# Kernel optimization log

Measured on AMD Instinct MI355X. Metric: run time of the kernel, lower is better.

## Reference

```python
import jax, jax.numpy as jnp
import numpy as np

NY = NX = 512
NSHOT = 4
NSRC = 2
NREC = 64
NT = 32
DX = 5.0          # grid spacing (m)
DT = 5e-4         # time step (s)
PML_WIDTH = 20
PML_FREQ = 25.0
MAX_VEL = 3500.0
C1, C2 = 9.0 / 8.0, -1.0 / 24.0  # 4th-order staggered FD coefficients


def _shift(p, axis, o, n):
    idx = [slice(None)] * p.ndim
    idx[axis] = slice(2 + o, 2 + o + n)
    return p[tuple(idx)]


def diff_plus(f, axis, d):
    # forward staggered derivative: value at half point between i and i+1
    n = f.shape[axis]
    pad = [(0, 0)] * f.ndim
    pad[axis] = (2, 2)
    p = jnp.pad(f, pad)
    return (C1 * (_shift(p, axis, 1, n) - _shift(p, axis, 0, n))
            + C2 * (_shift(p, axis, 2, n) - _shift(p, axis, -1, n))) / d


def diff_minus(f, axis, d):
    # backward staggered derivative
    n = f.shape[axis]
    pad = [(0, 0)] * f.ndim
    pad[axis] = (2, 2)
    p = jnp.pad(f, pad)
    return (C1 * (_shift(p, axis, 0, n) - _shift(p, axis, -1, n))
            + C2 * (_shift(p, axis, 1, n) - _shift(p, axis, -2, n))) / d


def pml_profiles(n):
    # C-PML coefficients a, b along one axis
    x = jnp.arange(n, dtype=jnp.float32)
    w = float(PML_WIDTH)
    frac = jnp.clip(jnp.maximum((w - x) / w, (x - (n - 1 - w)) / w), 0.0, 1.0)
    sigma = (3.0 * MAX_VEL * np.float32(np.log(1000.0)) / (2.0 * w * DX)) * frac ** 2
    alpha = np.float32(np.pi * PML_FREQ)
    b = jnp.exp(-(sigma + alpha) * DT)
    a = sigma / (sigma + alpha) * (b - 1.0)
    return a, b


def elastic_forward(lamb, mu, buoyancy, source_amplitudes_y,
                    source_locations_y, receiver_locations_y):
    ny, nx = lamb.shape
    nshot, nsrc, nt = source_amplitudes_y.shape
    ay, by = pml_profiles(ny)
    ax, bx = pml_profiles(nx)
    ay, by = ay[None, :, None], by[None, :, None]
    ax, bx = ax[None, None, :], bx[None, None, :]
    lam2mu = lamb + 2.0 * mu

    sb = jnp.arange(nshot)[:, None]
    sy, sx = source_locations_y[..., 0], source_locations_y[..., 1]
    ry, rx = receiver_locations_y[..., 0], receiver_locations_y[..., 1]
    src_scale = DT * buoyancy[sy, sx]  # [shot, nsrc]

    z = jnp.zeros((nshot, ny, nx), jnp.float32)
    fields0 = (z,) * 13  # vy, vx, syy, sxy, sxx + 8 PML memory fields

    def step(carry, amp_t):
        (vy, vx, syy, sxy, sxx,
         m_vyy, m_vyx, m_vxy, m_vxx,
         m_syyy, m_sxyy, m_sxyx, m_sxxx) = carry
        # --- velocity update from stress derivatives (with C-PML) ---
        dsyy = diff_minus(syy, 1, DX)
        m_syyy = by * m_syyy + ay * dsyy
        dsxy_x = diff_plus(sxy, 2, DX)
        m_sxyx = bx * m_sxyx + ax * dsxy_x
        vy = vy + DT * buoyancy * ((dsyy + m_syyy) + (dsxy_x + m_sxyx))
        dsxy_y = diff_plus(sxy, 1, DX)
        m_sxyy = by * m_sxyy + ay * dsxy_y
        dsxx = diff_minus(sxx, 2, DX)
        m_sxxx = bx * m_sxxx + ax * dsxx
        vx = vx + DT * buoyancy * ((dsxy_y + m_sxyy) + (dsxx + m_sxxx))
        # --- inject y-oriented velocity sources ---
        vy = vy.at[sb, sy, sx].add(amp_t * src_scale)
        # --- stress update from velocity derivatives (with C-PML) ---
        dvyy = diff_plus(vy, 1, DX)
        m_vyy = by * m_vyy + ay * dvyy
        dvxx = diff_plus(vx, 2, DX)
        m_vxx = bx * m_vxx + ax * dvxx
        tvyy, tvxx = dvyy + m_vyy, dvxx + m_vxx
        syy = syy + DT * (lam2mu * tvyy + lamb * tvxx)
        sxx = sxx + DT * (lam2mu * tvxx + lamb * tvyy)
        dvyx = diff_minus(vy, 2, DX)
        m_vyx = bx * m_vyx + ax * dvyx
        dvxy = diff_minus(vx, 1, DX)
        m_vxy = by * m_vxy + ay * dvxy
        sxy = sxy + DT * mu * ((dvyx + m_vyx) + (dvxy + m_vxy))
        rec = vy[sb, ry, rx]  # [shot, nrec]
        new = (vy, vx, syy, sxy, sxx, m_vyy, m_vyx, m_vxy, m_vxx,
               m_syyy, m_sxyy, m_sxyx, m_sxxx)
        return new, rec

    amps = jnp.moveaxis(source_amplitudes_y, -1, 0)  # [nt, shot, nsrc]
    _, recs = jax.lax.scan(jax.checkpoint(step), fields0, amps)
    return jnp.moveaxis(recs, 0, -1)  # [shot, nrec, nt]


def setup_inputs() -> dict:
    key = jax.random.key(0)
    k1, k2, k3, k4 = jax.random.split(key, 4)
    rho = 2200.0
    vp = 1500.0 + 2000.0 * jax.random.uniform(k1, (NY, NX), jnp.float32)
    vs = vp / 1.73
    mu = rho * vs ** 2
    lamb = rho * vp ** 2 - 2.0 * mu
    buoyancy = jnp.full((NY, NX), 1.0 / rho, jnp.float32)
    lo, hi = PML_WIDTH + 10, NY - PML_WIDTH - 10
    source_locations_y = jax.random.randint(k2, (NSHOT, NSRC, 2), lo, hi, jnp.int64)
    receiver_locations_y = jax.random.randint(k3, (NSHOT, NREC, 2), lo, hi, jnp.int64)
    source_amplitudes_y = jax.random.normal(k4, (NSHOT, NSRC, NT), jnp.float32) * 1e3
    return {"lamb": lamb, "mu": mu, "buoyancy": buoyancy,
            "source_amplitudes_y": source_amplitudes_y,
            "source_locations_y": source_locations_y,
            "receiver_locations_y": receiver_locations_y}


def reference(lamb, mu, buoyancy, source_amplitudes_y,
              source_locations_y, receiver_locations_y):
    return elastic_forward(lamb, mu, buoyancy, source_amplitudes_y,
                           source_locations_y, receiver_locations_y)
```

## Files before the change

### kernel.cpp

```cpp
#include <hip/hip_runtime.h>

#define NY 512
#define NX 512
#define NSHOT 4
#define NSRC 2
#define NREC 64
#define NT 32
#define DTF 0.0005f
#define PML_W 20
#define C1F 1.125f
#define C2F (-1.0f/24.0f)
#define INV_DX 0.2f

#define NXS 516
#define FSH (NY*NXS)

__device__ __forceinline__ bool in_pml(int i) {
    return (i < PML_W) | (i >= NY - PML_W);
}

__global__ void init_profiles(float* __restrict__ pa, float* __restrict__ pb) {
    int i = blockIdx.x * blockDim.x + threadIdx.x;
    if (i >= NY) return;
    float w = (float)PML_W;
    float x = (float)i;
    float frac = fmaxf((w - x) / w, (x - (float)(NY - 1 - PML_W)) / w);
    frac = fminf(fmaxf(frac, 0.0f), 1.0f);
    float sigma = 3.0f * 3500.0f * 6.9077553f / (2.0f * w * 5.0f) * frac * frac;
    float alpha = 78.539816f;
    float b = __expf(-(sigma + alpha) * DTF);
    pb[i] = b;
    pa[i] = sigma / (sigma + alpha) * (b - 1.0f);
}

__global__ void halo_zero(float* __restrict__ fields) {
    int i = blockIdx.x * blockDim.x + threadIdx.x;
    if (i >= 5 * NSHOT * NY * 4) return;
    int c   = i & 3;
    int r   = i >> 2;
    int row = r % NY;
    int fs  = r / NY;
    int col = (c < 2) ? c : 512 + c;
    fields[(size_t)fs * FSH + row * NXS + col] = 0.0f;
}

__device__ __forceinline__ void swizzle_block(int& s, int& y, int& xb) {
    int flat = (int)blockIdx.x + 2 * ((int)blockIdx.y + 512 * (int)blockIdx.z);
    int xcd   = flat & 7;
    int local = flat >> 3;
    int c = xcd * 512 + local;
    xb = c & 1;
    y  = (c >> 1) & 511;
    s  = c >> 10;
}

template<bool FIRST>
__global__ __launch_bounds__(256) void vel_kernel(
    const float* __restrict__ syy, const float* __restrict__ sxy, const float* __restrict__ sxx,
    float* __restrict__ vy, float* __restrict__ vx,
    float* __restrict__ m_syyy, float* __restrict__ m_sxyy,
    float* __restrict__ m_sxyx, float* __restrict__ m_sxxx,
    const float* __restrict__ buoy,
    const float* __restrict__ pa, const float* __restrict__ pb,
    const float* __restrict__ amps, const int* __restrict__ srcloc, int t)
{
    int s, y, xb;
    swizzle_block(s, y, xb);
    int x = xb * 256 + (int)threadIdx.x;
    int sbase = s * FSH;
    int idx = sbase + y * NXS + x + 2;

    const bool gm2 = !FIRST && (y >= 2);
    const bool gm1 = !FIRST && (y >= 1);
    const bool gp1 = !FIRST && (y <= NY - 2);
    const bool gp2 = !FIRST && (y <= NY - 3);

    float syy_0  = FIRST ? 0.0f : syy[idx];
    float syy_m1 = gm1 ? syy[idx - NXS] : 0.0f;
    float syy_m2 = gm2 ? syy[idx - 2 * NXS] : 0.0f;
    float syy_p1 = gp1 ? syy[idx + NXS] : 0.0f;
    float dsyy = (C1F * (syy_0 - syy_m1) + C2F * (syy_p1 - syy_m2)) * INV_DX;

    float sxy_0   = FIRST ? 0.0f : sxy[idx];
    float sxy_xm1 = FIRST ? 0.0f : sxy[idx - 1];
    float sxy_xp1 = FIRST ? 0.0f : sxy[idx + 1];
    float sxy_xp2 = FIRST ? 0.0f : sxy[idx + 2];
    float dsxy_x = (C1F * (sxy_xp1 - sxy_0) + C2F * (sxy_xp2 - sxy_xm1)) * INV_DX;

    float sxy_ym1 = gm1 ? sxy[idx - NXS] : 0.0f;
    float sxy_yp1 = gp1 ? sxy[idx + NXS] : 0.0f;
    float sxy_yp2 = gp2 ? sxy[idx + 2 * NXS] : 0.0f;
    float dsxy_y = (C1F * (sxy_yp1 - sxy_0) + C2F * (sxy_yp2 - sxy_ym1)) * INV_DX;

    float sxx_0   = FIRST ? 0.0f : sxx[idx];
    float sxx_xm1 = FIRST ? 0.0f : sxx[idx - 1];
    float sxx_xm2 = FIRST ? 0.0f : sxx[idx - 2];
    float sxx_xp1 = FIRST ? 0.0f : sxx[idx + 1];
    float dsxx = (C1F * (sxx_0 - sxx_xm1) + C2F * (sxx_xp1 - sxx_xm2)) * INV_DX;

    float msyyy = 0.0f, msxyy = 0.0f;
    if (in_pml(y)) {
        float ay = pa[y], by = pb[y];
        float mo1 = FIRST ? 0.0f : m_syyy[idx];
        float mo2 = FIRST ? 0.0f : m_sxyy[idx];
        msyyy = by * mo1 + ay * dsyy;   m_syyy[idx] = msyyy;
        msxyy = by * mo2 + ay * dsxy_y; m_sxyy[idx] = msxyy;
    }
    float msxyx = 0.0f, msxxx = 0.0f;
    if (in_pml(x)) {
        float ax = pa[x], bx = pb[x];
        float mo1 = FIRST ? 0.0f : m_sxyx[idx];
        float mo2 = FIRST ? 0.0f : m_sxxx[idx];
        msxyx = bx * mo1 + ax * dsxy_x; m_sxyx[idx] = msxyx;
        msxxx = bx * mo2 + ax * dsxx;   m_sxxx[idx] = msxxx;
    }

    float b = buoy[y * NX + x];
    float vyo = FIRST ? 0.0f : vy[idx];
    float vxo = FIRST ? 0.0f : vx[idx];
    float vy_new = vyo + DTF * b * ((dsyy + msyyy) + (dsxy_x + msxyx));
    vx[idx] = vxo + DTF * b * ((dsxy_y + msxyy) + (dsxx + msxxx));

#pragma unroll
    for (int i = 0; i < NSRC; ++i) {
        int sy = srcloc[(s * NSRC + i) * 2 + 0];
        int sx = srcloc[(s * NSRC + i) * 2 + 1];
        if (sy == y && sx == x) {
            vy_new += amps[(s * NSRC + i) * NT + t] * DTF * b;
        }
    }
    vy[idx] = vy_new;
}

template<bool FIRST>
__global__ __launch_bounds__(256) void stress_kernel(
    const float* __restrict__ vy, const float* __restrict__ vx,
    float* __restrict__ syy, float* __restrict__ sxy, float* __restrict__ sxx,
    float* __restrict__ m_vyy, float* __restrict__ m_vyx,
    float* __restrict__ m_vxy, float* __restrict__ m_vxx,
    const float* __restrict__ lamb, const float* __restrict__ mu,
    const float* __restrict__ pa, const float* __restrict__ pb,
    const int* __restrict__ recloc, float* __restrict__ out, int t)
{
    int s, y, xb;
    swizzle_block(s, y, xb);
    int x = xb * 256 + (int)threadIdx.x;
    int sbase = s * FSH;
    int idx = sbase + y * NXS + x + 2;

    if (blockIdx.x == 0 && blockIdx.y == 0 && blockIdx.z == 0) {
        int p = threadIdx.x;
        if (p < NSHOT * NREC) {
            int sh = p / NREC;
            int ry = recloc[p * 2 + 0];
            int rx = recloc[p * 2 + 1];
            out[p * NT + t] = vy[sh * FSH + ry * NXS + rx + 2];
        }
    }

    const bool gm2 = (y >= 2);
    const bool gm1 = (y >= 1);
    const bool gp1 = (y <= NY - 2);
    const bool gp2 = (y <= NY - 3);

    float vy_0   = vy[idx];
    float vy_ym1 = gm1 ? vy[idx - NXS] : 0.0f;
    float vy_yp1 = gp1 ? vy[idx + NXS] : 0.0f;
    float vy_yp2 = gp2 ? vy[idx + 2 * NXS] : 0.0f;
    float dvyy = (C1F * (vy_yp1 - vy_0) + C2F * (vy_yp2 - vy_ym1)) * INV_DX;

    float vx_0   = vx[idx];
    float vx_xm1 = vx[idx - 1];
    float vx_xp1 = vx[idx + 1];
    float vx_xp2 = vx[idx + 2];
    float dvxx = (C1F * (vx_xp1 - vx_0) + C2F * (vx_xp2 - vx_xm1)) * INV_DX;

    float vy_xm1 = vy[idx - 1];
    float vy_xm2 = vy[idx - 2];
    float vy_xp1 = vy[idx + 1];
    float dvyx = (C1F * (vy_0 - vy_xm1) + C2F * (vy_xp1 - vy_xm2)) * INV_DX;

    float vx_ym1 = gm1 ? vx[idx - NXS] : 0.0f;
    float vx_ym2 = gm2 ? vx[idx - 2 * NXS] : 0.0f;
    float vx_yp1 = gp1 ? vx[idx + NXS] : 0.0f;
    float dvxy = (C1F * (vx_0 - vx_ym1) + C2F * (vx_yp1 - vx_ym2)) * INV_DX;

    float mvyy = 0.0f, mvxy = 0.0f;
    if (in_pml(y)) {
        float ay = pa[y], by = pb[y];
        float mo1 = FIRST ? 0.0f : m_vyy[idx];
        float mo2 = FIRST ? 0.0f : m_vxy[idx];
        mvyy = by * mo1 + ay * dvyy; m_vyy[idx] = mvyy;
        mvxy = by * mo2 + ay * dvxy; m_vxy[idx] = mvxy;
    }
    float mvxx = 0.0f, mvyx = 0.0f;
    if (in_pml(x)) {
        float ax = pa[x], bx = pb[x];
        float mo1 = FIRST ? 0.0f : m_vxx[idx];
        float mo2 = FIRST ? 0.0f : m_vyx[idx];
        mvxx = bx * mo1 + ax * dvxx; m_vxx[idx] = mvxx;
        mvyx = bx * mo2 + ax * dvyx; m_vyx[idx] = mvyx;
    }

    float tvyy = dvyy + mvyy;
    float tvxx = dvxx + mvxx;

    float la = lamb[y * NX + x];
    float m  = mu[y * NX + x];
    float l2m = la + 2.0f * m;
    float syyo = FIRST ? 0.0f : syy[idx];
    float sxxo = FIRST ? 0.0f : sxx[idx];
    float sxyo = FIRST ? 0.0f : sxy[idx];
    syy[idx] = syyo + DTF * (l2m * tvyy + la * tvxx);
    sxx[idx] = sxxo + DTF * (l2m * tvxx + la * tvyy);
    sxy[idx] = sxyo + DTF * m * ((dvyx + mvyx) + (dvxy + mvxy));
}

extern "C" void kernel_launch(void* const* d_in, const int* in_sizes, int n_in,
                              void* d_out, int out_size, void* d_ws, size_t ws_size,
                              hipStream_t stream) {
    const float* lamb   = (const float*)d_in[0];
    const float* mu     = (const float*)d_in[1];
    const float* buoy   = (const float*)d_in[2];
    const float* amps   = (const float*)d_in[3];
    const int*   srcloc = (const int*)d_in[4];
    const int*   recloc = (const int*)d_in[5];
    float* out = (float*)d_out;

    float* ws = (float*)d_ws;
    float* pa = ws;
    float* pb = ws + 512;
    const size_t F = (size_t)NSHOT * FSH;
    float* fields = ws + 1024;
    float* vy     = fields + 0  * F;
    float* vx     = fields + 1  * F;
    float* syy    = fields + 2  * F;
    float* sxy    = fields + 3  * F;
    float* sxx    = fields + 4  * F;
    float* m_vyy  = fields + 5  * F;
    float* m_vyx  = fields + 6  * F;
    float* m_vxy  = fields + 7  * F;
    float* m_vxx  = fields + 8  * F;
    float* m_syyy = fields + 9  * F;
    float* m_sxyy = fields + 10 * F;
    float* m_sxyx = fields + 11 * F;
    float* m_sxxx = fields + 12 * F;

    init_profiles<<<2, 256, 0, stream>>>(pa, pb);
    halo_zero<<<(5 * NSHOT * NY * 4 + 255) / 256, 256, 0, stream>>>(fields);

    dim3 grid(NX / 256, NY, NSHOT);
    dim3 block(256);
    vel_kernel<true><<<grid, block, 0, stream>>>(syy, sxy, sxx, vy, vx,
                                                 m_syyy, m_sxyy, m_sxyx, m_sxxx,
                                                 buoy, pa, pb, amps, srcloc, 0);
    stress_kernel<true><<<grid, block, 0, stream>>>(vy, vx, syy, sxy, sxx,
                                                    m_vyy, m_vyx, m_vxy, m_vxx,
                                                    lamb, mu, pa, pb, recloc, out, 0);
    for (int t = 1; t < NT; ++t) {
        vel_kernel<false><<<grid, block, 0, stream>>>(syy, sxy, sxx, vy, vx,
                                                      m_syyy, m_sxyy, m_sxyx, m_sxxx,
                                                      buoy, pa, pb, amps, srcloc, t);
        stress_kernel<false><<<grid, block, 0, stream>>>(vy, vx, syy, sxy, sxx,
                                                         m_vyy, m_vyx, m_vxy, m_vxx,
                                                         lamb, mu, pa, pb, recloc, out, t);
    }
}
```

Before: 492.9 us.

## Fuse all time steps into one persistent cooperative kernel with grid syncs

Replaces the 64 separate velocity/stress kernel launches with a single cooperative persistent kernel of 1024 blocks. Each block handles four row-chunks, and the kernel uses grid.sync() between the velocity and stress phases of every time step. The goal is to remove per-launch overhead and the kernel-boundary drains. In exchange it pays for 64 grid-wide barriers and needs 4 resident blocks per CU. If the occupancy check fails, it falls back to the multi-launch path.

```diff
diff --git a/kernel.cpp b/kernel.cpp
--- a/kernel.cpp
+++ b/kernel.cpp
@@ -1,4 +1,7 @@
 #include <hip/hip_runtime.h>
+#include <hip/hip_cooperative_groups.h>
+
+namespace cg = cooperative_groups;
 
 #define NY 512
 #define NX 512
@@ -44,31 +47,19 @@
     fields[(size_t)fs * FSH + row * NXS + col] = 0.0f;
 }
 
-__device__ __forceinline__ void swizzle_block(int& s, int& y, int& xb) {
-    int flat = (int)blockIdx.x + 2 * ((int)blockIdx.y + 512 * (int)blockIdx.z);
-    int xcd   = flat & 7;
-    int local = flat >> 3;
-    int c = xcd * 512 + local;
-    xb = c & 1;
-    y  = (c >> 1) & 511;
-    s  = c >> 10;
-}
 
 template<bool FIRST>
-__global__ __launch_bounds__(256) void vel_kernel(
+__device__ __forceinline__ void vel_point(
     const float* __restrict__ syy, const float* __restrict__ sxy, const float* __restrict__ sxx,
     float* __restrict__ vy, float* __restrict__ vx,
     float* __restrict__ m_syyy, float* __restrict__ m_sxyy,
     float* __restrict__ m_sxyx, float* __restrict__ m_sxxx,
     const float* __restrict__ buoy,
     const float* __restrict__ pa, const float* __restrict__ pb,
-    const float* __restrict__ amps, const int* __restrict__ srcloc, int t)
-{
-    int s, y, xb;
-    swizzle_block(s, y, xb);
-    int x = xb * 256 + (int)threadIdx.x;
-    int sbase = s * FSH;
-    int idx = sbase + y * NXS + x + 2;
+    const float* __restrict__ amps, const int* __restrict__ srcloc,
+    int t, int s, int y, int x)
+{
+    int idx = s * FSH + y * NXS + x + 2;
 
     const bool gm2 = !FIRST && (y >= 2);
     const bool gm1 = !FIRST && (y >= 1);
@@ -133,30 +124,16 @@
 }
 
 template<bool FIRST>
-__global__ __launch_bounds__(256) void stress_kernel(
+__device__ __forceinline__ void stress_point(
     const float* __restrict__ vy, const float* __restrict__ vx,
     float* __restrict__ syy, float* __restrict__ sxy, float* __restrict__ sxx,
     float* __restrict__ m_vyy, float* __restrict__ m_vyx,
     float* __restrict__ m_vxy, float* __restrict__ m_vxx,
     const float* __restrict__ lamb, const float* __restrict__ mu,
     const float* __restrict__ pa, const float* __restrict__ pb,
-    const int* __restrict__ recloc, float* __restrict__ out, int t)
-{
-    int s, y, xb;
-    swizzle_block(s, y, xb);
-    int x = xb * 256 + (int)threadIdx.x;
-    int sbase = s * FSH;
-    int idx = sbase + y * NXS + x + 2;
-
-    if (blockIdx.x == 0 && blockIdx.y == 0 && blockIdx.z == 0) {
-        int p = threadIdx.x;
-        if (p < NSHOT * NREC) {
-            int sh = p / NREC;
-            int ry = recloc[p * 2 + 0];
-            int rx = recloc[p * 2 + 1];
-            out[p * NT + t] = vy[sh * FSH + ry * NXS + rx + 2];
-        }
-    }
+    int s, int y, int x)
+{
+    int idx = s * FSH + y * NXS + x + 2;
 
     const bool gm2 = (y >= 2);
     const bool gm1 = (y >= 1);
@@ -214,6 +191,120 @@
     syy[idx] = syyo + DTF * (l2m * tvyy + la * tvxx);
     sxx[idx] = sxxo + DTF * (l2m * tvxx + la * tvyy);
     sxy[idx] = sxyo + DTF * m * ((dvyx + mvyx) + (dvxy + mvxy));
+}
+
+__global__ __launch_bounds__(256, 4) void sim_kernel(
+    float* __restrict__ vy, float* __restrict__ vx,
+    float* __restrict__ syy, float* __restrict__ sxy, float* __restrict__ sxx,
+    float* __restrict__ m_syyy, float* __restrict__ m_sxyy,
+    float* __restrict__ m_sxyx, float* __restrict__ m_sxxx,
+    float* __restrict__ m_vyy, float* __restrict__ m_vyx,
+    float* __restrict__ m_vxy, float* __restrict__ m_vxx,
+    const float* __restrict__ buoy, const float* __restrict__ lamb,
+    const float* __restrict__ mu,
+    const float* __restrict__ pa, const float* __restrict__ pb,
+    const float* __restrict__ amps, const int* __restrict__ srcloc,
+    const int* __restrict__ recloc, float* __restrict__ out)
+{
+    cg::grid_group grid = cg::this_grid();
+    const int b    = (int)blockIdx.x;
+    const int base = (b & 7) * 512 + (b >> 3) * 4;
+    const int tid  = (int)threadIdx.x;
+
+    for (int t = 0; t < NT; ++t) {
+        if (t == 0) {
+            for (int k = 0; k < 4; ++k) {
+                int c = base + k;
+                vel_point<true>(syy, sxy, sxx, vy, vx, m_syyy, m_sxyy, m_sxyx, m_sxxx,
+                                buoy, pa, pb, amps, srcloc, t,
+                                c >> 10, (c >> 1) & 511, (c & 1) * 256 + tid);
+            }
+        } else {
+            for (int k = 0; k < 4; ++k) {
+                int c = base + k;
+                vel_point<false>(syy, sxy, sxx, vy, vx, m_syyy, m_sxyy, m_sxyx, m_sxxx,
+                                 buoy, pa, pb, amps, srcloc, t,
+                                 c >> 10, (c >> 1) & 511, (c & 1) * 256 + tid);
+            }
+        }
+        grid.sync();
+
+        if (b == 0 && tid < NSHOT * NREC) {
+            int sh = tid / NREC;
+            int ry = recloc[tid * 2 + 0];
+            int rx = recloc[tid * 2 + 1];
+            out[tid * NT + t] = vy[sh * FSH + ry * NXS + rx + 2];
+        }
+
+        if (t == 0) {
+            for (int k = 0; k < 4; ++k) {
+                int c = base + k;
+                stress_point<true>(vy, vx, syy, sxy, sxx, m_vyy, m_vyx, m_vxy, m_vxx,
+                                   lamb, mu, pa, pb,
+                                   c >> 10, (c >> 1) & 511, (c & 1) * 256 + tid);
+            }
+        } else {
+            for (int k = 0; k < 4; ++k) {
+                int c = base + k;
+                stress_point<false>(vy, vx, syy, sxy, sxx, m_vyy, m_vyx, m_vxy, m_vxx,
+                                    lamb, mu, pa, pb,
+                                    c >> 10, (c >> 1) & 511, (c & 1) * 256 + tid);
+            }
+        }
+        grid.sync();
+    }
+}
+
+
+__device__ __forceinline__ void swizzle_block(int& s, int& y, int& xb) {
+    int flat = (int)blockIdx.x + 2 * ((int)blockIdx.y + 512 * (int)blockIdx.z);
+    int xcd   = flat & 7;
+    int local = flat >> 3;
+    int c = xcd * 512 + local;
+    xb = c & 1;
+    y  = (c >> 1) & 511;
+    s  = c >> 10;
+}
+
+template<bool FIRST>
+__global__ __launch_bounds__(256) void vel_kernel(
+    const float* __restrict__ syy, const float* __restrict__ sxy, const float* __restrict__ sxx,
+    float* __restrict__ vy, float* __restrict__ vx,
+    float* __restrict__ m_syyy, float* __restrict__ m_sxyy,
+    float* __restrict__ m_sxyx, float* __restrict__ m_sxxx,
+    const float* __restrict__ buoy,
+    const float* __restrict__ pa, const float* __restrict__ pb,
+    const float* __restrict__ amps, const int* __restrict__ srcloc, int t)
+{
+    int s, y, xb;
+    swizzle_block(s, y, xb);
+    vel_point<FIRST>(syy, sxy, sxx, vy, vx, m_syyy, m_sxyy, m_sxyx, m_sxxx,
+                     buoy, pa, pb, amps, srcloc, t, s, y, xb * 256 + (int)threadIdx.x);
+}
+
+template<bool FIRST>
+__global__ __launch_bounds__(256) void stress_kernel(
+    const float* __restrict__ vy, const float* __restrict__ vx,
+    float* __restrict__ syy, float* __restrict__ sxy, float* __restrict__ sxx,
+    float* __restrict__ m_vyy, float* __restrict__ m_vyx,
+    float* __restrict__ m_vxy, float* __restrict__ m_vxx,
+    const float* __restrict__ lamb, const float* __restrict__ mu,
+    const float* __restrict__ pa, const float* __restrict__ pb,
+    const int* __restrict__ recloc, float* __restrict__ out, int t)
+{
+    int s, y, xb;
+    swizzle_block(s, y, xb);
+    if (blockIdx.x == 0 && blockIdx.y == 0 && blockIdx.z == 0) {
+        int p = threadIdx.x;
+        if (p < NSHOT * NREC) {
+            int sh = p / NREC;
+            int ry = recloc[p * 2 + 0];
+            int rx = recloc[p * 2 + 1];
+            out[p * NT + t] = vy[sh * FSH + ry * NXS + rx + 2];
+        }
+    }
+    stress_point<FIRST>(vy, vx, syy, sxy, sxx, m_vyy, m_vyx, m_vxy, m_vxx,
+                        lamb, mu, pa, pb, s, y, xb * 256 + (int)threadIdx.x);
 }
 
 extern "C" void kernel_launch(void* const* d_in, const int* in_sizes, int n_in,
@@ -249,20 +340,41 @@
     init_profiles<<<2, 256, 0, stream>>>(pa, pb);
     halo_zero<<<(5 * NSHOT * NY * 4 + 255) / 256, 256, 0, stream>>>(fields);
 
-    dim3 grid(NX / 256, NY, NSHOT);
-    dim3 block(256);
-    vel_kernel<true><<<grid, block, 0, stream>>>(syy, sxy, sxx, vy, vx,
-                                                 m_syyy, m_sxyy, m_sxyx, m_sxxx,
-                                                 buoy, pa, pb, amps, srcloc, 0);
-    stress_kernel<true><<<grid, block, 0, stream>>>(vy, vx, syy, sxy, sxx,
-                                                    m_vyy, m_vyx, m_vxy, m_vxx,
-                                                    lamb, mu, pa, pb, recloc, out, 0);
-    for (int t = 1; t < NT; ++t) {
-        vel_kernel<false><<<grid, block, 0, stream>>>(syy, sxy, sxx, vy, vx,
-                                                      m_syyy, m_sxyy, m_sxyx, m_sxxx,
-                                                      buoy, pa, pb, amps, srcloc, t);
-        stress_kernel<false><<<grid, block, 0, stream>>>(vy, vx, syy, sxy, sxx,
-                                                         m_vyy, m_vyx, m_vxy, m_vxx,
-                                                         lamb, mu, pa, pb, recloc, out, t);
-    }
-}
+    static int coop_ok = -1;
+    if (coop_ok < 0) {
+        int maxb = 0;
+        hipError_t e = hipOccupancyMaxActiveBlocksPerMultiprocessor(
+            &maxb, reinterpret_cast<const void*>(sim_kernel), 256, 0);
+        coop_ok = (e == hipSuccess && maxb >= 4) ? 1 : 0;
+    }
+
+    if (coop_ok) {
+        void* args[] = {
+            (void*)&vy, (void*)&vx, (void*)&syy, (void*)&sxy, (void*)&sxx,
+            (void*)&m_syyy, (void*)&m_sxyy, (void*)&m_sxyx, (void*)&m_sxxx,
+            (void*)&m_vyy, (void*)&m_vyx, (void*)&m_vxy, (void*)&m_vxx,
+            (void*)&buoy, (void*)&lamb, (void*)&mu,
+            (void*)&pa, (void*)&pb,
+            (void*)&amps, (void*)&srcloc, (void*)&recloc, (void*)&out
+        };
+        hipLaunchCooperativeKernel(reinterpret_cast<const void*>(sim_kernel),
+                                   dim3(1024), dim3(256), args, 0, stream);
+    } else {
+        dim3 grid(NX / 256, NY, NSHOT);
+        dim3 block(256);
+        vel_kernel<true><<<grid, block, 0, stream>>>(syy, sxy, sxx, vy, vx,
+                                                     m_syyy, m_sxyy, m_sxyx, m_sxxx,
+                                                     buoy, pa, pb, amps, srcloc, 0);
+        stress_kernel<true><<<grid, block, 0, stream>>>(vy, vx, syy, sxy, sxx,
+                                                        m_vyy, m_vyx, m_vxy, m_vxx,
+                                                        lamb, mu, pa, pb, recloc, out, 0);
+        for (int t = 1; t < NT; ++t) {
+            vel_kernel<false><<<grid, block, 0, stream>>>(syy, sxy, sxx, vy, vx,
+                                                          m_syyy, m_sxyy, m_sxyx, m_sxxx,
+                                                          buoy, pa, pb, amps, srcloc, t);
+            stress_kernel<false><<<grid, block, 0, stream>>>(vy, vx, syy, sxy, sxx,
+                                                             m_vyy, m_vyx, m_vxy, m_vxx,
+                                                             lamb, mu, pa, pb, recloc, out, t);
+        }
+    }
+}
```

Result: no change. 490.6 us (-0.5%).

## Skip blocks outside source light cone and zero all fields with memset

Applied to the files above, without the earlier changes.

Each velocity and stress block first checks whether its row and x-range lie within a growing radius (4 cells per step plus a margin) of any source in its shot, and exits early if not. This avoids reading and writing wavefield and PML arrays that are still exactly zero early in the simulation. To make skipped regions valid, all 13 field arrays are now zeroed with a memset up front, replacing the halo-only zeroing and the FIRST template specialisation. The trade-off is the cost of the full memset and a small per-block gating check.

```diff
diff --git a/kernel.cpp b/kernel.cpp
--- a/kernel.cpp
+++ b/kernel.cpp
@@ -33,17 +33,6 @@
     pa[i] = sigma / (sigma + alpha) * (b - 1.0f);
 }
 
-__global__ void halo_zero(float* __restrict__ fields) {
-    int i = blockIdx.x * blockDim.x + threadIdx.x;
-    if (i >= 5 * NSHOT * NY * 4) return;
-    int c   = i & 3;
-    int r   = i >> 2;
-    int row = r % NY;
-    int fs  = r / NY;
-    int col = (c < 2) ? c : 512 + c;
-    fields[(size_t)fs * FSH + row * NXS + col] = 0.0f;
-}
-
 __device__ __forceinline__ void swizzle_block(int& s, int& y, int& xb) {
     int flat = (int)blockIdx.x + 2 * ((int)blockIdx.y + 512 * (int)blockIdx.z);
     int xcd   = flat & 7;
@@ -54,7 +43,19 @@
     s  = c >> 10;
 }
 
-template<bool FIRST>
+__device__ __forceinline__ bool cone_active(const int* __restrict__ srcloc,
+                                            int s, int y, int xb, int R) {
+    int xlo = xb * 256, xhi = xlo + 255;
+    bool act = false;
+#pragma unroll
+    for (int i = 0; i < NSRC; ++i) {
+        int sy = srcloc[(s * NSRC + i) * 2 + 0];
+        int sx = srcloc[(s * NSRC + i) * 2 + 1];
+        act |= (abs(y - sy) <= R) & (sx + R >= xlo) & (sx - R <= xhi);
+    }
+    return act;
+}
+
 __global__ __launch_bounds__(256) void vel_kernel(
     const float* __restrict__ syy, const float* __restrict__ sxy, const float* __restrict__ sxx,
     float* __restrict__ vy, float* __restrict__ vx,
@@ -66,25 +67,26 @@
 {
     int s, y, xb;
     swizzle_block(s, y, xb);
+    if (!cone_active(srcloc, s, y, xb, 4 * t + 6)) return;
+
     int x = xb * 256 + (int)threadIdx.x;
-    int sbase = s * FSH;
-    int idx = sbase + y * NXS + x + 2;
-
-    const bool gm2 = !FIRST && (y >= 2);
-    const bool gm1 = !FIRST && (y >= 1);
-    const bool gp1 = !FIRST && (y <= NY - 2);
-    const bool gp2 = !FIRST && (y <= NY - 3);
-
-    float syy_0  = FIRST ? 0.0f : syy[idx];
+    int idx = s * FSH + y * NXS + x + 2;
+
+    const bool gm2 = (y >= 2);
+    const bool gm1 = (y >= 1);
+    const bool gp1 = (y <= NY - 2);
+    const bool gp2 = (y <= NY - 3);
+
+    float syy_0  = syy[idx];
     float syy_m1 = gm1 ? syy[idx - NXS] : 0.0f;
     float syy_m2 = gm2 ? syy[idx - 2 * NXS] : 0.0f;
     float syy_p1 = gp1 ? syy[idx + NXS] : 0.0f;
     float dsyy = (C1F * (syy_0 - syy_m1) + C2F * (syy_p1 - syy_m2)) * INV_DX;
 
-    float sxy_0   = FIRST ? 0.0f : sxy[idx];
-    float sxy_xm1 = FIRST ? 0.0f : sxy[idx - 1];
-    float sxy_xp1 = FIRST ? 0.0f : sxy[idx + 1];
-    float sxy_xp2 = FIRST ? 0.0f : sxy[idx + 2];
+    float sxy_0   = sxy[idx];
+    float sxy_xm1 = sxy[idx - 1];
+    float sxy_xp1 = sxy[idx + 1];
+    float sxy_xp2 = sxy[idx + 2];
     float dsxy_x = (C1F * (sxy_xp1 - sxy_0) + C2F * (sxy_xp2 - sxy_xm1)) * INV_DX;
 
     float sxy_ym1 = gm1 ? sxy[idx - NXS] : 0.0f;
@@ -92,34 +94,28 @@
     float sxy_yp2 = gp2 ? sxy[idx + 2 * NXS] : 0.0f;
     float dsxy_y = (C1F * (sxy_yp1 - sxy_0) + C2F * (sxy_yp2 - sxy_ym1)) * INV_DX;
 
-    float sxx_0   = FIRST ? 0.0f : sxx[idx];
-    float sxx_xm1 = FIRST ? 0.0f : sxx[idx - 1];
-    float sxx_xm2 = FIRST ? 0.0f : sxx[idx - 2];
-    float sxx_xp1 = FIRST ? 0.0f : sxx[idx + 1];
+    float sxx_0   = sxx[idx];
+    float sxx_xm1 = sxx[idx - 1];
+    float sxx_xm2 = sxx[idx - 2];
+    float sxx_xp1 = sxx[idx + 1];
     float dsxx = (C1F * (sxx_0 - sxx_xm1) + C2F * (sxx_xp1 - sxx_xm2)) * INV_DX;
 
     float msyyy = 0.0f, msxyy = 0.0f;
     if (in_pml(y)) {
         float ay = pa[y], by = pb[y];
-        float mo1 = FIRST ? 0.0f : m_syyy[idx];
-        float mo2 = FIRST ? 0.0f : m_sxyy[idx];
-        msyyy = by * mo1 + ay * dsyy;   m_syyy[idx] = msyyy;
-        msxyy = by * mo2 + ay * dsxy_y; m_sxyy[idx] = msxyy;
+        msyyy = by * m_syyy[idx] + ay * dsyy;   m_syyy[idx] = msyyy;
+        msxyy = by * m_sxyy[idx] + ay * dsxy_y; m_sxyy[idx] = msxyy;
     }
     float msxyx = 0.0f, msxxx = 0.0f;
     if (in_pml(x)) {
         float ax = pa[x], bx = pb[x];
-        float mo1 = FIRST ? 0.0f : m_sxyx[idx];
-        float mo2 = FIRST ? 0.0f : m_sxxx[idx];
-        msxyx = bx * mo1 + ax * dsxy_x; m_sxyx[idx] = msxyx;
-        msxxx = bx * mo2 + ax * dsxx;   m_sxxx[idx] = msxxx;
+        msxyx = bx * m_sxyx[idx] + ax * dsxy_x; m_sxyx[idx] = msxyx;
+        msxxx = bx * m_sxxx[idx] + ax * dsxx;   m_sxxx[idx] = msxxx;
     }
 
     float b = buoy[y * NX + x];
-    float vyo = FIRST ? 0.0f : vy[idx];
-    float vxo = FIRST ? 0.0f : vx[idx];
-    float vy_new = vyo + DTF * b * ((dsyy + msyyy) + (dsxy_x + msxyx));
-    vx[idx] = vxo + DTF * b * ((dsxy_y + msxyy) + (dsxx + msxxx));
+    float vy_new = vy[idx] + DTF * b * ((dsyy + msyyy) + (dsxy_x + msxyx));
+    vx[idx] += DTF * b * ((dsxy_y + msxyy) + (dsxx + msxxx));
 
 #pragma unroll
     for (int i = 0; i < NSRC; ++i) {
@@ -132,21 +128,18 @@
     vy[idx] = vy_new;
 }
 
-template<bool FIRST>
-__global__ __launch_bounds__(256) void stress_kernel(
+__global__ __launch_bounds__(256) void stress_kernel_gated(
     const float* __restrict__ vy, const float* __restrict__ vx,
     float* __restrict__ syy, float* __restrict__ sxy, float* __restrict__ sxx,
     float* __restrict__ m_vyy, float* __restrict__ m_vyx,
     float* __restrict__ m_vxy, float* __restrict__ m_vxx,
     const float* __restrict__ lamb, const float* __restrict__ mu,
     const float* __restrict__ pa, const float* __restrict__ pb,
-    const int* __restrict__ recloc, float* __restrict__ out, int t)
+    const int* __restrict__ recloc, float* __restrict__ out,
+    const int* __restrict__ srcloc, int t)
 {
     int s, y, xb;
     swizzle_block(s, y, xb);
-    int x = xb * 256 + (int)threadIdx.x;
-    int sbase = s * FSH;
-    int idx = sbase + y * NXS + x + 2;
 
     if (blockIdx.x == 0 && blockIdx.y == 0 && blockIdx.z == 0) {
         int p = threadIdx.x;
@@ -157,6 +150,10 @@
             out[p * NT + t] = vy[sh * FSH + ry * NXS + rx + 2];
         }
     }
+    if (!cone_active(srcloc, s, y, xb, 4 * t + 8)) return;
+
+    int x = xb * 256 + (int)threadIdx.x;
+    int idx = s * FSH + y * NXS + x + 2;
 
     const bool gm2 = (y >= 2);
     const bool gm1 = (y >= 1);
@@ -188,18 +185,14 @@
     float mvyy = 0.0f, mvxy = 0.0f;
     if (in_pml(y)) {
         float ay = pa[y], by = pb[y];
-        float mo1 = FIRST ? 0.0f : m_vyy[idx];
-        float mo2 = FIRST ? 0.0f : m_vxy[idx];
-        mvyy = by * mo1 + ay * dvyy; m_vyy[idx] = mvyy;
-        mvxy = by * mo2 + ay * dvxy; m_vxy[idx] = mvxy;
+        mvyy = by * m_vyy[idx] + ay * dvyy; m_vyy[idx] = mvyy;
+        mvxy = by * m_vxy[idx] + ay * dvxy; m_vxy[idx] = mvxy;
     }
     float mvxx = 0.0f, mvyx = 0.0f;
     if (in_pml(x)) {
         float ax = pa[x], bx = pb[x];
-        float mo1 = FIRST ? 0.0f : m_vxx[idx];
-        float mo2 = FIRST ? 0.0f : m_vyx[idx];
-        mvxx = bx * mo1 + ax * dvxx; m_vxx[idx] = mvxx;
-        mvyx = bx * mo2 + ax * dvyx; m_vyx[idx] = mvyx;
+        mvxx = bx * m_vxx[idx] + ax * dvxx; m_vxx[idx] = mvxx;
+        mvyx = bx * m_vyx[idx] + ax * dvyx; m_vyx[idx] = mvyx;
     }
 
     float tvyy = dvyy + mvyy;
@@ -208,12 +201,9 @@
     float la = lamb[y * NX + x];
     float m  = mu[y * NX + x];
     float l2m = la + 2.0f * m;
-    float syyo = FIRST ? 0.0f : syy[idx];
-    float sxxo = FIRST ? 0.0f : sxx[idx];
-    float sxyo = FIRST ? 0.0f : sxy[idx];
-    syy[idx] = syyo + DTF * (l2m * tvyy + la * tvxx);
-    sxx[idx] = sxxo + DTF * (l2m * tvxx + la * tvyy);
-    sxy[idx] = sxyo + DTF * m * ((dvyx + mvyx) + (dvxy + mvxy));
+    syy[idx] += DTF * (l2m * tvyy + la * tvxx);
+    sxx[idx] += DTF * (l2m * tvxx + la * tvyy);
+    sxy[idx] += DTF * m * ((dvyx + mvyx) + (dvxy + mvxy));
 }
 
 extern "C" void kernel_launch(void* const* d_in, const int* in_sizes, int n_in,
@@ -246,23 +236,18 @@
     float* m_sxyx = fields + 11 * F;
     float* m_sxxx = fields + 12 * F;
 
+    (void)hipMemsetAsync(fields, 0, 13 * F * sizeof(float), stream);
     init_profiles<<<2, 256, 0, stream>>>(pa, pb);
-    halo_zero<<<(5 * NSHOT * NY * 4 + 255) / 256, 256, 0, stream>>>(fields);
 
     dim3 grid(NX / 256, NY, NSHOT);
     dim3 block(256);
-    vel_kernel<true><<<grid, block, 0, stream>>>(syy, sxy, sxx, vy, vx,
-                                                 m_syyy, m_sxyy, m_sxyx, m_sxxx,
-                                                 buoy, pa, pb, amps, srcloc, 0);
-    stress_kernel<true><<<grid, block, 0, stream>>>(vy, vx, syy, sxy, sxx,
-                                                    m_vyy, m_vyx, m_vxy, m_vxx,
-                                                    lamb, mu, pa, pb, recloc, out, 0);
-    for (int t = 1; t < NT; ++t) {
-        vel_kernel<false><<<grid, block, 0, stream>>>(syy, sxy, sxx, vy, vx,
-                                                      m_syyy, m_sxyy, m_sxyx, m_sxxx,
-                                                      buoy, pa, pb, amps, srcloc, t);
-        stress_kernel<false><<<grid, block, 0, stream>>>(vy, vx, syy, sxy, sxx,
-                                                         m_vyy, m_vyx, m_vxy, m_vxx,
-                                                         lamb, mu, pa, pb, recloc, out, t);
-    }
-}
+    for (int t = 0; t < NT; ++t) {
+        vel_kernel<<<grid, block, 0, stream>>>(syy, sxy, sxx, vy, vx,
+                                               m_syyy, m_sxyy, m_sxyx, m_sxxx,
+                                               buoy, pa, pb, amps, srcloc, t);
+        stress_kernel_gated<<<grid, block, 0, stream>>>(vy, vx, syy, sxy, sxx,
+                                                        m_vyy, m_vyx, m_vxy, m_vxx,
+                                                        lamb, mu, pa, pb, recloc, out,
+                                                        srcloc, t);
+    }
+}
```

New measurement: 433.5 us. -12.0%, faster.
